# Kernel optimization log

Measured on AMD Instinct MI355X. Metric: run time of the kernel, lower is better.

## Reference

```python
import jax, jax.numpy as jnp
import numpy as np

G, N, E = 2048, 64, 256      # graphs, nodes/graph, edges/graph
NHID = 64
RATIO = 0.5
K = int(np.ceil(RATIO * N))  # SAGPooling keep count = 32
P = 200000                   # ddi edges


def setup_inputs() -> dict:
    key = jax.random.key(0)
    ks = jax.random.split(key, 9)
    graph_edges = jax.random.randint(ks[0], (G, 2, E), 0, N)
    ddi_edge_index = jax.random.randint(ks[1], (2, P), 0, G)
    s = 1.0 / np.sqrt(NHID)
    return {
        "graph_edges": graph_edges,
        "ddi_edge_index": ddi_edge_index,
        # GCNConv(1 -> nhid)
        "conv1_w": jax.random.normal(ks[2], (1, NHID), jnp.float32) * 1.0,
        "conv1_b": jnp.zeros((NHID,), jnp.float32),
        # SAGPooling score GNN: GraphConv(nhid -> 1)
        "sag_w_rel": jax.random.normal(ks[3], (NHID, 1), jnp.float32) * s,
        "sag_b_rel": jnp.zeros((1,), jnp.float32),
        "sag_w_root": jax.random.normal(ks[4], (NHID, 1), jnp.float32) * s,
        # pred_layer: Linear(4*nhid -> 1)
        "pred_w": jax.random.normal(ks[5], (4 * NHID, 1), jnp.float32) * (1.0 / np.sqrt(4 * NHID)),
        "pred_b": jnp.zeros((1,), jnp.float32),
    }


def _per_graph(edges, conv1_w, conv1_b, sag_w_rel, sag_b_rel, sag_w_root):
    # edges: [2, E] int
    src, dst = edges[0], edges[1]
    w = jnp.ones((E,), jnp.float32)  # edge_weight = 1.0
    # --- GCNConv(1 -> nhid) with added self loops ---
    deg = jnp.zeros((N,), jnp.float32).at[dst].add(w) + 1.0  # self-loop weight 1
    dinv = deg ** -0.5
    xw = jnp.broadcast_to(conv1_w[0], (N, NHID))  # ones(N,1) @ W
    norm = dinv[src] * w * dinv[dst]              # [E]
    h = jnp.zeros((N, NHID), jnp.float32).at[dst].add(xw[src] * norm[:, None])
    h = h + xw / deg[:, None] + conv1_b           # self-loop norm = 1/deg
    h = jax.nn.relu(h)
    # --- SAGPooling: GraphConv score + top-k + tanh gating ---
    aggr = jnp.zeros((N, NHID), jnp.float32).at[dst].add(h[src] * w[:, None])
    score = (aggr @ sag_w_rel + sag_b_rel + h @ sag_w_root)[:, 0]  # [N]
    vals, idx = jax.lax.top_k(score, K)
    xp = h[idx] * jnp.tanh(vals)[:, None]         # [K, nhid]
    # --- global max pool || global mean pool ---
    return jnp.concatenate([xp.max(axis=0), xp.mean(axis=0)])  # [2*nhid]


def reference(graph_edges, ddi_edge_index, conv1_w, conv1_b, sag_w_rel,
              sag_b_rel, sag_w_root, pred_w, pred_b):
    mod_feat = jax.vmap(_per_graph, in_axes=(0, None, None, None, None, None))(
        graph_edges, conv1_w, conv1_b, sag_w_rel, sag_b_rel, sag_w_root)  # [G, 2*nhid]
    # dropout: identity (deterministic / eval reference)
    s, d = ddi_edge_index[0], ddi_edge_index[1]
    ef = jnp.concatenate([mod_feat[s], mod_feat[d]], axis=1)  # [P, 4*nhid]
    return jax.nn.sigmoid(ef @ pred_w + pred_b)[:, 0]          # [P]
```

## Files before the change

kernel.cpp:

```cpp
#include <hip/hip_runtime.h>
#include <math.h>

constexpr int NN  = 64;
constexpr int EE  = 256;
constexpr int NH  = 64;
constexpr int KK  = 32;

__global__ __launch_bounds__(64) void graph_feat_kernel(
    const int*   __restrict__ graph_edges,
    const float* __restrict__ conv1_w,
    const float* __restrict__ conv1_b,
    const float* __restrict__ wrel,
    const float* __restrict__ brel,
    const float* __restrict__ wroot,
    const float* __restrict__ pred_w,
    float*       __restrict__ ab)
{
    const int g    = blockIdx.x;
    const int lane = threadIdx.x;

    __shared__ int   s_src[EE];
    __shared__ int   s_dst[EE];
    __shared__ float s_deg[NN];
    __shared__ float s_dinv[NN];
    __shared__ float s_acc[NN];
    __shared__ float s_t[NN];
    __shared__ float s_score[NN];
    __shared__ float s_tanh[NN];
    __shared__ int   s_keep[NN];
    __shared__ float s_w[NH], s_b[NH], s_wr[NH], s_wo[NH];

    s_w[lane]  = conv1_w[lane];
    s_b[lane]  = conv1_b[lane];
    s_wr[lane] = wrel[lane];
    s_wo[lane] = wroot[lane];

    const int* eg = graph_edges + (size_t)g * 2 * EE;
    #pragma unroll
    for (int i = 0; i < 4; ++i) {
        s_src[lane + 64 * i] = eg[lane + 64 * i];
        s_dst[lane + 64 * i] = eg[EE + lane + 64 * i];
    }
    s_deg[lane] = 1.0f;
    s_acc[lane] = 0.0f;
    __syncthreads();

    #pragma unroll
    for (int i = 0; i < 4; ++i)
        atomicAdd(&s_deg[s_dst[lane + 64 * i]], 1.0f);
    __syncthreads();

    const float deg  = s_deg[lane];
    const float dinv = 1.0f / sqrtf(deg);
    s_dinv[lane] = dinv;
    __syncthreads();

    #pragma unroll
    for (int i = 0; i < 4; ++i) {
        const int e = lane + 64 * i;
        atomicAdd(&s_acc[s_dst[e]], s_dinv[s_src[e]]);
    }
    __syncthreads();

    const float c = s_acc[lane] * dinv + 1.0f / deg;
    s_acc[lane] = c;

    float t = 0.0f, u = 0.0f;
    for (int j = 0; j < NH; ++j) {
        const float h = fmaxf(s_w[j] * c + s_b[j], 0.0f);
        t = fmaf(h, s_wr[j], t);
        u = fmaf(h, s_wo[j], u);
    }
    s_t[lane] = t;
    s_score[lane] = u + brel[0];
    __syncthreads();

    #pragma unroll
    for (int i = 0; i < 4; ++i) {
        const int e = lane + 64 * i;
        atomicAdd(&s_score[s_dst[e]], s_t[s_src[e]]);
    }
    __syncthreads();

    const float score = s_score[lane];
    int rank = 0;
    for (int m = 0; m < NN; ++m) {
        const float sm = s_score[m];
        rank += (sm > score) || (sm == score && m < lane);
    }
    const int keep = (rank < KK) ? 1 : 0;
    s_keep[lane] = keep;
    s_tanh[lane] = keep ? tanhf(score) : 0.0f;
    __syncthreads();

    const float wj = s_w[lane], bj = s_b[lane];
    float fmx = -INFINITY, fsum = 0.0f;
    for (int n = 0; n < NN; ++n) {
        if (s_keep[n]) {
            const float h = fmaxf(wj * s_acc[n] + bj, 0.0f);
            const float v = h * s_tanh[n];
            fmx  = fmaxf(fmx, v);
            fsum += v;
        }
    }
    const float fmean = fsum * (1.0f / KK);

    float pa = fmx * pred_w[lane]       + fmean * pred_w[64 + lane];
    float pb = fmx * pred_w[128 + lane] + fmean * pred_w[192 + lane];
    #pragma unroll
    for (int off = 32; off > 0; off >>= 1) {
        pa += __shfl_down(pa, off);
        pb += __shfl_down(pb, off);
    }
    if (lane == 0) {
        ab[2 * g]     = pa;
        ab[2 * g + 1] = pb;
    }
}

__global__ __launch_bounds__(256) void pred_kernel(
    const int*   __restrict__ ddi,
    const float* __restrict__ ab,
    const float* __restrict__ pred_b,
    float*       __restrict__ out,
    int P)
{
    const int p = blockIdx.x * blockDim.x + threadIdx.x;
    if (p >= P) return;
    const int s = ddi[p];
    const int d = ddi[P + p];
    const float x = ab[2 * s] + ab[2 * d + 1] + pred_b[0];
    out[p] = 1.0f / (1.0f + __expf(-x) * 0.0f + expf(-x) * 1.0f);
}

extern "C" void kernel_launch(void* const* d_in, const int* in_sizes, int n_in,
                              void* d_out, int out_size, void* d_ws, size_t ws_size,
                              hipStream_t stream) {
    const int*   graph_edges = (const int*)  d_in[0];
    const int*   ddi         = (const int*)  d_in[1];
    const float* conv1_w     = (const float*)d_in[2];
    const float* conv1_b     = (const float*)d_in[3];
    const float* wrel        = (const float*)d_in[4];
    const float* brel        = (const float*)d_in[5];
    const float* wroot       = (const float*)d_in[6];
    const float* pred_w      = (const float*)d_in[7];
    const float* pred_b      = (const float*)d_in[8];
    float*       out         = (float*)d_out;

    const int G = in_sizes[0] / (2 * EE);
    const int P = in_sizes[1] / 2;

    float* ab = (float*)d_ws;

    graph_feat_kernel<<<G, 64, 0, stream>>>(
        graph_edges, conv1_w, conv1_b, wrel, brel, wroot, pred_w, ab);

    pred_kernel<<<(P + 255) / 256, 256, 0, stream>>>(
        ddi, ab, pred_b, out, P);
}
```

Measured before the change: 24.48 us.

## Keep per-graph data in registers with wave shuffles and vectorize edge/pred loads

The graph kernel now loads each lane's four edges as int4 into registers instead of staging them in shared memory. Weight broadcasts, the rank computation and the pooling loop use wave shuffles and a ballot mask, which removes several shared arrays and one barrier. The prediction kernel handles two edges per thread with int2 and float2 accesses and drops the redundant second exponential. Vector loads require aligned inputs, and the two-per-thread pred kernel assumes P is even.

```diff
diff --git a/kernel.cpp b/kernel.cpp
--- a/kernel.cpp
+++ b/kernel.cpp
@@ -3,7 +3,6 @@
 
 constexpr int NN  = 64;
 constexpr int EE  = 256;
-constexpr int NH  = 64;
 constexpr int KK  = 32;
 
 __global__ __launch_bounds__(64) void graph_feat_kernel(
@@ -19,35 +18,34 @@
     const int g    = blockIdx.x;
     const int lane = threadIdx.x;
 
-    __shared__ int   s_src[EE];
-    __shared__ int   s_dst[EE];
     __shared__ float s_deg[NN];
     __shared__ float s_dinv[NN];
     __shared__ float s_acc[NN];
     __shared__ float s_t[NN];
     __shared__ float s_score[NN];
-    __shared__ float s_tanh[NN];
-    __shared__ int   s_keep[NN];
-    __shared__ float s_w[NH], s_b[NH], s_wr[NH], s_wo[NH];
 
-    s_w[lane]  = conv1_w[lane];
-    s_b[lane]  = conv1_b[lane];
-    s_wr[lane] = wrel[lane];
-    s_wo[lane] = wroot[lane];
+    const float wj  = conv1_w[lane];
+    const float bj  = conv1_b[lane];
+    const float wrj = wrel[lane];
+    const float woj = wroot[lane];
+    const float pw0 = pred_w[lane];
+    const float pw1 = pred_w[64 + lane];
+    const float pw2 = pred_w[128 + lane];
+    const float pw3 = pred_w[192 + lane];
+    const float br  = brel[0];
 
     const int* eg = graph_edges + (size_t)g * 2 * EE;
-    #pragma unroll
-    for (int i = 0; i < 4; ++i) {
-        s_src[lane + 64 * i] = eg[lane + 64 * i];
-        s_dst[lane + 64 * i] = eg[EE + lane + 64 * i];
-    }
+    const int4 src4 = ((const int4*)eg)[lane];
+    const int4 dst4 = ((const int4*)(eg + EE))[lane];
+
     s_deg[lane] = 1.0f;
     s_acc[lane] = 0.0f;
     __syncthreads();
 
-    #pragma unroll
-    for (int i = 0; i < 4; ++i)
-        atomicAdd(&s_deg[s_dst[lane + 64 * i]], 1.0f);
+    atomicAdd(&s_deg[dst4.x], 1.0f);
+    atomicAdd(&s_deg[dst4.y], 1.0f);
+    atomicAdd(&s_deg[dst4.z], 1.0f);
+    atomicAdd(&s_deg[dst4.w], 1.0f);
     __syncthreads();
 
     const float deg  = s_deg[lane];
@@ -55,66 +53,69 @@
     s_dinv[lane] = dinv;
     __syncthreads();
 
-    #pragma unroll
-    for (int i = 0; i < 4; ++i) {
-        const int e = lane + 64 * i;
-        atomicAdd(&s_acc[s_dst[e]], s_dinv[s_src[e]]);
-    }
+    atomicAdd(&s_acc[dst4.x], s_dinv[src4.x]);
+    atomicAdd(&s_acc[dst4.y], s_dinv[src4.y]);
+    atomicAdd(&s_acc[dst4.z], s_dinv[src4.z]);
+    atomicAdd(&s_acc[dst4.w], s_dinv[src4.w]);
     __syncthreads();
 
     const float c = s_acc[lane] * dinv + 1.0f / deg;
-    s_acc[lane] = c;
 
     float t = 0.0f, u = 0.0f;
-    for (int j = 0; j < NH; ++j) {
-        const float h = fmaxf(s_w[j] * c + s_b[j], 0.0f);
-        t = fmaf(h, s_wr[j], t);
-        u = fmaf(h, s_wo[j], u);
+    #pragma unroll 16
+    for (int j = 0; j < 64; ++j) {
+        const float w_ = __shfl(wj,  j);
+        const float b_ = __shfl(bj,  j);
+        const float r_ = __shfl(wrj, j);
+        const float o_ = __shfl(woj, j);
+        const float h  = fmaxf(fmaf(w_, c, b_), 0.0f);
+        t = fmaf(h, r_, t);
+        u = fmaf(h, o_, u);
     }
-    s_t[lane] = t;
-    s_score[lane] = u + brel[0];
+    s_t[lane]     = t;
+    s_score[lane] = u + br;
     __syncthreads();
 
-    #pragma unroll
-    for (int i = 0; i < 4; ++i) {
-        const int e = lane + 64 * i;
-        atomicAdd(&s_score[s_dst[e]], s_t[s_src[e]]);
-    }
+    atomicAdd(&s_score[dst4.x], s_t[src4.x]);
+    atomicAdd(&s_score[dst4.y], s_t[src4.y]);
+    atomicAdd(&s_score[dst4.z], s_t[src4.z]);
+    atomicAdd(&s_score[dst4.w], s_t[src4.w]);
     __syncthreads();
 
-    const float score = s_score[lane];
+    const float sc = s_score[lane];
+
     int rank = 0;
-    for (int m = 0; m < NN; ++m) {
-        const float sm = s_score[m];
-        rank += (sm > score) || (sm == score && m < lane);
+    #pragma unroll 16
+    for (int m = 0; m < 64; ++m) {
+        const float sm = __shfl(sc, m);
+        rank += (sm > sc) || (sm == sc && m < lane);
     }
-    const int keep = (rank < KK) ? 1 : 0;
-    s_keep[lane] = keep;
-    s_tanh[lane] = keep ? tanhf(score) : 0.0f;
-    __syncthreads();
+    const int keep = rank < KK;
+    const float th = keep ? tanhf(sc) : 0.0f;
+    const unsigned long long kmask = __ballot(keep);
 
-    const float wj = s_w[lane], bj = s_b[lane];
     float fmx = -INFINITY, fsum = 0.0f;
-    for (int n = 0; n < NN; ++n) {
-        if (s_keep[n]) {
-            const float h = fmaxf(wj * s_acc[n] + bj, 0.0f);
-            const float v = h * s_tanh[n];
+    #pragma unroll 8
+    for (int n = 0; n < 64; ++n) {
+        if ((kmask >> n) & 1ull) {
+            const float cn = __shfl(c,  n);
+            const float tn = __shfl(th, n);
+            const float v  = fmaxf(fmaf(wj, cn, bj), 0.0f) * tn;
             fmx  = fmaxf(fmx, v);
             fsum += v;
         }
     }
     const float fmean = fsum * (1.0f / KK);
 
-    float pa = fmx * pred_w[lane]       + fmean * pred_w[64 + lane];
-    float pb = fmx * pred_w[128 + lane] + fmean * pred_w[192 + lane];
+    float pa = fmx * pw0 + fmean * pw1;
+    float pb = fmx * pw2 + fmean * pw3;
     #pragma unroll
     for (int off = 32; off > 0; off >>= 1) {
-        pa += __shfl_down(pa, off);
-        pb += __shfl_down(pb, off);
+        pa += __shfl_xor(pa, off);
+        pb += __shfl_xor(pb, off);
     }
     if (lane == 0) {
-        ab[2 * g]     = pa;
-        ab[2 * g + 1] = pb;
+        ((float2*)ab)[g] = make_float2(pa, pb);
     }
 }
 
@@ -123,14 +124,19 @@
     const float* __restrict__ ab,
     const float* __restrict__ pred_b,
     float*       __restrict__ out,
-    int P)
+    int P2)
 {
-    const int p = blockIdx.x * blockDim.x + threadIdx.x;
-    if (p >= P) return;
-    const int s = ddi[p];
-    const int d = ddi[P + p];
-    const float x = ab[2 * s] + ab[2 * d + 1] + pred_b[0];
-    out[p] = 1.0f / (1.0f + __expf(-x) * 0.0f + expf(-x) * 1.0f);
+    const int p2 = blockIdx.x * blockDim.x + threadIdx.x;
+    if (p2 >= P2) return;
+    const float pb = pred_b[0];
+    const int2 s2 = ((const int2*)ddi)[p2];
+    const int2 d2 = ((const int2*)ddi)[P2 + p2];
+    const float x0 = ab[2 * s2.x] + ab[2 * d2.x + 1] + pb;
+    const float x1 = ab[2 * s2.y] + ab[2 * d2.y + 1] + pb;
+    float2 o;
+    o.x = 1.0f / (1.0f + expf(-x0));
+    o.y = 1.0f / (1.0f + expf(-x1));
+    ((float2*)out)[p2] = o;
 }
 
 extern "C" void kernel_launch(void* const* d_in, const int* in_sizes, int n_in,
@@ -155,6 +161,6 @@
     graph_feat_kernel<<<G, 64, 0, stream>>>(
         graph_edges, conv1_w, conv1_b, wrel, brel, wroot, pred_w, ab);
 
-    pred_kernel<<<(P + 255) / 256, 256, 0, stream>>>(
-        ddi, ab, pred_b, out, P);
+    const int P2 = P / 2;
+    pred_kernel<<<(P2 + 255) / 256, 256, 0, stream>>>(ddi, ab, pred_b, out, P2);
 }
```

Result: slower. 27.98 us (+14.3%).
